# Kernel optimization log

Measured on AMD Instinct MI355X. Metric: run time of the kernel, lower is better.

The kernel has to match this reference:

```python
import jax, jax.numpy as jnp
import numpy as np

N_FEATURES = 40
H = 64
N_CLASSES = 3
N_NODES = 100000
N_EDGES = 3200000
THRESHOLD = 0.5


def setup_inputs() -> dict:
    key = jax.random.key(0)
    ks = jax.random.split(key, 8)
    x = jax.random.normal(ks[0], (N_NODES, N_FEATURES), dtype=jnp.float32)
    edge_index = jax.random.randint(ks[1], (2, N_EDGES), 0, N_NODES, dtype=jnp.int64)
    s1 = 1.0 / np.sqrt(N_FEATURES)
    s2 = 1.0 / np.sqrt(H)
    W1 = jax.random.uniform(ks[2], (N_FEATURES, H), jnp.float32, -s1, s1)
    b1 = jnp.zeros((H,), jnp.float32)
    Wf = jax.random.uniform(ks[3], (H, H), jnp.float32, -s2, s2)
    bf = jax.random.uniform(ks[4], (H,), jnp.float32, -s2, s2)
    W2 = jax.random.uniform(ks[5], (H, N_CLASSES), jnp.float32, -s2, s2)
    b2 = jnp.zeros((N_CLASSES,), jnp.float32)
    ethical_filter = jnp.ones((N_CLASSES,), jnp.float32)
    return {"x": x, "edge_index": edge_index, "W1": W1, "b1": b1,
            "Wf": Wf, "bf": bf, "W2": W2, "b2": b2,
            "ethical_filter": ethical_filter}


def _gcn_conv(x, W, b, src, dst, n_nodes):
    # PyG GCNConv: add self-loops, symmetric normalization, src->dst aggregate.
    h = x @ W                                   # [N, F_out]
    loop = jnp.arange(n_nodes, dtype=src.dtype)
    s = jnp.concatenate([src, loop])            # [E+N]
    d = jnp.concatenate([dst, loop])
    deg = jnp.zeros((n_nodes,), h.dtype).at[d].add(1.0)
    dinv = jax.lax.rsqrt(deg)                   # deg >= 1 due to self-loops
    norm = dinv[s] * dinv[d]                    # [E+N]
    msg = h[s] * norm[:, None]                  # gather + scale
    out = jnp.zeros((n_nodes, h.shape[1]), h.dtype).at[d].add(msg)
    return out + b


def reference(x, edge_index, W1, b1, Wf, bf, W2, b2, ethical_filter):
    n = x.shape[0]
    src, dst = edge_index[0], edge_index[1]
    h = jax.nn.relu(_gcn_conv(x, W1, b1, src, dst, n))
    # SpikingNeuron: mem = fc(h); spike = (mem >= threshold).float()
    spike = (h @ Wf + bf >= THRESHOLD).astype(x.dtype)
    out = _gcn_conv(spike, W2, b2, src, dst, n)
    return out * ethical_filter
```

## Files before the change

### kernel.cpp

```cpp
#include <hip/hip_runtime.h>

#define NF 40
#define NF4 10
#define H  64
#define NC 3
#define BK 256
#define CAP 10240
#define MAXNBK 512
#define SMASK 0xFFFFFu
#define NSLC 16
#define SSH 13

typedef float floatx4 __attribute__((ext_vector_type(4)));

__global__ void k_zero(int* __restrict__ p, int n) {
    int i = blockIdx.x * blockDim.x + threadIdx.x;
    if (i < n) p[i] = 0;
}

__global__ __launch_bounds__(1024) void k_bin(const int* __restrict__ src,
                                              const int* __restrict__ dst,
                                              int* __restrict__ gcur,
                                              unsigned* __restrict__ staging,
                                              int ne, int nbk) {
    __shared__ int lh[MAXNBK];
    __shared__ int lcur[MAXNBK];
    int t = threadIdx.x;
    for (int b = t; b < nbk; b += 1024) lh[b] = 0;
    __syncthreads();
    int gtid = blockIdx.x * 1024 + t;
    int NT = gridDim.x * 1024;
    int bk[13]; unsigned ed[13];
    #pragma unroll
    for (int u = 0; u < 13; ++u) {
        int i = gtid + u * NT;
        bool v = (i < ne);
        int dv = v ? dst[i] : 0;
        int sv = v ? src[i] : 0;
        bk[u] = v ? (dv >> 8) : -1;
        ed[u] = ((unsigned)(dv & 255) << 20) | (unsigned)sv;
        if (v) atomicAdd(&lh[dv >> 8], 1);
    }
    for (int i = gtid + 13 * NT; i < ne; i += NT)
        atomicAdd(&lh[dst[i] >> 8], 1);
    __syncthreads();
    for (int b = t; b < nbk; b += 1024)
        lcur[b] = lh[b] ? atomicAdd(&gcur[b], lh[b]) : 0;
    __syncthreads();
    #pragma unroll
    for (int u = 0; u < 13; ++u) {
        if (bk[u] >= 0) {
            int p = atomicAdd(&lcur[bk[u]], 1);
            staging[(size_t)bk[u] * CAP + p] = ed[u];
        }
    }
    for (int i = gtid + 13 * NT; i < ne; i += NT) {
        int dv = dst[i], sv = src[i]; int b = dv >> 8;
        int p = atomicAdd(&lcur[b], 1);
        staging[(size_t)b * CAP + p] = ((unsigned)(dv & 255) << 20) | (unsigned)sv;
    }
}

__global__ __launch_bounds__(512) void k_sort(unsigned* __restrict__ staging,
                                              const int* __restrict__ gcur,
                                              int* __restrict__ rs, int* __restrict__ rl,
                                              float* __restrict__ dinv, int n) {
    __shared__ unsigned buf[CAP];
    __shared__ int cnt[BK * NSLC];
    __shared__ int tsum[512];
    int b = blockIdx.x, t = threadIdx.x;
    int ebase = b * CAP;
    int rlen = gcur[b];
    for (int j = t; j < rlen; j += 512) buf[j] = staging[ebase + j];
    for (int i = t; i < BK * NSLC; i += 512) cnt[i] = 0;
    __syncthreads();
    for (int j = t; j < rlen; j += 512) {
        unsigned e = buf[j];
        int key = ((int)(e >> 20) << 4) | (int)((e & SMASK) >> SSH);
        atomicAdd(&cnt[key], 1);
    }
    __syncthreads();
    int base8 = t * 8;
    int loc[8]; int run = 0;
    #pragma unroll
    for (int i = 0; i < 8; ++i) { loc[i] = run; run += cnt[base8 + i]; }
    tsum[t] = run;
    __syncthreads();
    for (int off = 1; off < 512; off <<= 1) {
        int a = (t >= off) ? tsum[t - off] : 0;
        __syncthreads();
        tsum[t] += a;
        __syncthreads();
    }
    int texcl = tsum[t] - run;
    #pragma unroll
    for (int i = 0; i < 8; ++i) cnt[base8 + i] = texcl + loc[i];
    __syncthreads();
    if (t < BK) {
        int node = b * BK + t;
        int st0 = cnt[t * NSLC];
        int en0 = (t == BK - 1) ? rlen : cnt[(t + 1) * NSLC];
        int deg = en0 - st0;
        if (node < n) {
            rs[node] = ebase + st0;
            rl[node] = deg;
            dinv[node] = rsqrtf((float)(deg + 1));
        }
    }
    __syncthreads();
    for (int j = t; j < rlen; j += 512) {
        unsigned e = buf[j];
        int key = ((int)(e >> 20) << 4) | (int)((e & SMASK) >> SSH);
        int p = atomicAdd(&cnt[key], 1);
        staging[ebase + p] = e;
    }
}

__global__ __launch_bounds__(256) void k_pull1(
        const unsigned* __restrict__ st, const int* __restrict__ rs,
        const int* __restrict__ rl, const float* __restrict__ dinv,
        const float4* __restrict__ x4, float* __restrict__ ax, int n) {
    __shared__ float4 red[4][64];
    int t = threadIdx.x;
    int w = t >> 6, lane = t & 63;
    int d = blockIdx.x * 4 + w;
    if (d >= n) return;
    int g = lane / 10, f = lane - g * 10;
    int beg = rs[d], len = rl[d];
    float dd = dinv[d];
    float4 acc = make_float4(0.f, 0.f, 0.f, 0.f);
    if (g < 6) {
        int j = beg + g, end = beg + len;
        for (; j + 6 < end; j += 12) {
            unsigned eA = __builtin_nontemporal_load(st + j);
            unsigned eB = __builtin_nontemporal_load(st + j + 6);
            int sA = (int)(eA & SMASK), sB = (int)(eB & SMASK);
            float wA = dinv[sA], wB = dinv[sB];
            float4 a4 = x4[sA * NF4 + f];
            float4 b4 = x4[sB * NF4 + f];
            acc.x += a4.x * wA + b4.x * wB;
            acc.y += a4.y * wA + b4.y * wB;
            acc.z += a4.z * wA + b4.z * wB;
            acc.w += a4.w * wA + b4.w * wB;
        }
        if (j < end) {
            unsigned e = __builtin_nontemporal_load(st + j);
            int s = (int)(e & SMASK);
            float wv = dinv[s];
            float4 v = x4[s * NF4 + f];
            acc.x += v.x * wv; acc.y += v.y * wv;
            acc.z += v.z * wv; acc.w += v.w * wv;
        }
    }
    red[w][lane] = acc;
    if (lane < NF4) {
        float4 tot = red[w][lane];
        #pragma unroll
        for (int gg = 1; gg < 6; ++gg) {
            float4 r = red[w][gg * 10 + lane];
            tot.x += r.x; tot.y += r.y; tot.z += r.z; tot.w += r.w;
        }
        float4 self = x4[d * NF4 + lane];
        floatx4 o;
        o.x = dd * (tot.x + self.x * dd);
        o.y = dd * (tot.y + self.y * dd);
        o.z = dd * (tot.z + self.z * dd);
        o.w = dd * (tot.w + self.w * dd);
        __builtin_nontemporal_store(o, (floatx4*)(ax + (size_t)d * NF + 4 * lane));
    }
}

__global__ __launch_bounds__(256, 2) void k_node(
        const float4* __restrict__ ax4,
        const float* __restrict__ W1, const float* __restrict__ b1,
        const float* __restrict__ Wf, const float* __restrict__ bf,
        const float* __restrict__ W2, const float* __restrict__ dinv,
        float4* __restrict__ s2sp4, int n) {
    __shared__ float lW1[NF * H];
    __shared__ float lWf[H * H];
    __shared__ float hT[4][H * 32];
    int t = threadIdx.x, w = t >> 6, lane = t & 63;
    int r = lane & 7, c = lane >> 3;

    for (int i = t; i < NF * H; i += 256) lW1[i] = W1[i];
    for (int i = t; i < H * H;  i += 256) lWf[i] = Wf[i];
    __syncthreads();

    int nb0 = (blockIdx.x * 4 + w) * 32;
    if (nb0 >= n) return;
    int cnt = min(32, n - nb0);

    float bb[8], bfv[8], w2s[8][3];
    #pragma unroll
    for (int j = 0; j < 8; ++j) {
        bb[j]  = b1[8 * c + j];
        bfv[j] = bf[8 * c + j];
        w2s[j][0] = W2[(8 * c + j) * NC + 0];
        w2s[j][1] = W2[(8 * c + j) * NC + 1];
        w2s[j][2] = W2[(8 * c + j) * NC + 2];
    }

    float* axT = &hT[w][0];
    #pragma unroll
    for (int i = 0; i < 5; ++i) {
        int idx = lane + 64 * i;
        int no = idx / NF4, q = idx - no * NF4;
        float4 a = make_float4(0.f, 0.f, 0.f, 0.f);
        if (no < cnt) a = ax4[(size_t)(nb0 + no) * NF4 + q];
        axT[(4 * q + 0) * 32 + no] = a.x;
        axT[(4 * q + 1) * 32 + no] = a.y;
        axT[(4 * q + 2) * 32 + no] = a.z;
        axT[(4 * q + 3) * 32 + no] = a.w;
    }

    float acc[4][8];
    #pragma unroll
    for (int i = 0; i < 4; ++i)
        #pragma unroll
        for (int j = 0; j < 8; ++j) acc[i][j] = bb[j];
    for (int k = 0; k < NF; ++k) {
        float4 a   = *(const float4*)&axT[k * 32 + 4 * r];
        float4 blo = *(const float4*)&lW1[k * H + 8 * c];
        float4 bhi = *(const float4*)&lW1[k * H + 8 * c + 4];
        float av[4] = {a.x, a.y, a.z, a.w};
        float bv[8] = {blo.x, blo.y, blo.z, blo.w, bhi.x, bhi.y, bhi.z, bhi.w};
        #pragma unroll
        for (int i = 0; i < 4; ++i)
            #pragma unroll
            for (int j = 0; j < 8; ++j) acc[i][j] = fmaf(av[i], bv[j], acc[i][j]);
    }
    #pragma unroll
    for (int j = 0; j < 8; ++j) {
        float4 hv = make_float4(fmaxf(acc[0][j], 0.f), fmaxf(acc[1][j], 0.f),
                                fmaxf(acc[2][j], 0.f), fmaxf(acc[3][j], 0.f));
        *(float4*)&hT[w][(8 * c + j) * 32 + 4 * r] = hv;
    }

    float acc2[4][8];
    #pragma unroll
    for (int i = 0; i < 4; ++i)
        #pragma unroll
        for (int j = 0; j < 8; ++j) acc2[i][j] = bfv[j];
    for (int k = 0; k < H; ++k) {
        float4 a   = *(const float4*)&hT[w][k * 32 + 4 * r];
        float4 blo = *(const float4*)&lWf[k * H + 8 * c];
        float4 bhi = *(const float4*)&lWf[k * H + 8 * c + 4];
        float av[4] = {a.x, a.y, a.z, a.w};
        float bv[8] = {blo.x, blo.y, blo.z, blo.w, bhi.x, bhi.y, bhi.z, bhi.w};
        #pragma unroll
        for (int i = 0; i < 4; ++i)
            #pragma unroll
            for (int j = 0; j < 8; ++j) acc2[i][j] = fmaf(av[i], bv[j], acc2[i][j]);
    }

    float p0[4], p1[4], p2[4];
    #pragma unroll
    for (int i = 0; i < 4; ++i) { p0[i] = 0.f; p1[i] = 0.f; p2[i] = 0.f; }
    #pragma unroll
    for (int i = 0; i < 4; ++i)
        #pragma unroll
        for (int j = 0; j < 8; ++j) {
            float s = (acc2[i][j] >= 0.5f) ? 1.f : 0.f;
            p0[i] = fmaf(s, w2s[j][0], p0[i]);
            p1[i] = fmaf(s, w2s[j][1], p1[i]);
            p2[i] = fmaf(s, w2s[j][2], p2[i]);
        }
    #pragma unroll
    for (int off = 8; off < 64; off <<= 1) {
        #pragma unroll
        for (int i = 0; i < 4; ++i) {
            p0[i] += __shfl_xor(p0[i], off);
            p1[i] += __shfl_xor(p1[i], off);
            p2[i] += __shfl_xor(p2[i], off);
        }
    }
    if (c == 0) {
        #pragma unroll
        for (int i = 0; i < 4; ++i) {
            int no = 4 * r + i;
            if (no < cnt) {
                int node = nb0 + no;
                float di = dinv[node];
                s2sp4[node] = make_float4(p0[i] * di, p1[i] * di, p2[i] * di, 0.f);
            }
        }
    }
}

__global__ __launch_bounds__(256) void k_pull2(
        const unsigned* __restrict__ st, const int* __restrict__ rs,
        const int* __restrict__ rl, const float* __restrict__ dinv,
        const float4* __restrict__ s2sp4, const float* __restrict__ b2,
        const float* __restrict__ ef, float* __restrict__ out, int n) {
    int t = threadIdx.x;
    int w = t >> 6, lane = t & 63;
    int d = blockIdx.x * 4 + w;
    if (d >= n) return;
    int beg = rs[d], end = beg + rl[d];
    float a0 = 0.f, a1 = 0.f, a2 = 0.f;
    for (int j = beg + lane; j < end; j += 64) {
        unsigned e = __builtin_nontemporal_load(st + j);
        float4 v = s2sp4[e & SMASK];
        a0 += v.x; a1 += v.y; a2 += v.z;
    }
    for (int off = 32; off; off >>= 1) {
        a0 += __shfl_down(a0, off);
        a1 += __shfl_down(a1, off);
        a2 += __shfl_down(a2, off);
    }
    if (lane == 0) {
        float dd = dinv[d];
        float4 self = s2sp4[d];
        out[d * NC + 0] = (dd * (a0 + self.x) + b2[0]) * ef[0];
        out[d * NC + 1] = (dd * (a1 + self.y) + b2[1]) * ef[1];
        out[d * NC + 2] = (dd * (a2 + self.z) + b2[2]) * ef[2];
    }
}

extern "C" void kernel_launch(void* const* d_in, const int* in_sizes, int n_in,
                              void* d_out, int out_size, void* d_ws, size_t ws_size,
                              hipStream_t stream) {
    const float* x  = (const float*)d_in[0];
    const int*   ei = (const int*)d_in[1];
    const float* W1 = (const float*)d_in[2];
    const float* b1 = (const float*)d_in[3];
    const float* Wf = (const float*)d_in[4];
    const float* bf = (const float*)d_in[5];
    const float* W2 = (const float*)d_in[6];
    const float* b2 = (const float*)d_in[7];
    const float* ef = (const float*)d_in[8];

    int n  = in_sizes[0] / NF;
    int ne = in_sizes[1] / 2;
    const int* src = ei;
    const int* dst = ei + ne;
    int nbk = (n + BK - 1) >> 8;

    auto al = [](size_t v) { return (v + 255) & ~(size_t)255; };
    char* ws = (char*)d_ws;
    size_t off = 0;
    unsigned* staging = (unsigned*)(ws + off); off += al((size_t)nbk * CAP * 4);
    float*    axbuf   = (float*)(ws + off);    off += al((size_t)n * NF * 4);
    float*    s2sp    = (float*)(ws + off);    off += al((size_t)n * 4 * 4);
    float*    dinv    = (float*)(ws + off);    off += al((size_t)n * 4);
    int*      rsb     = (int*)(ws + off);      off += al((size_t)n * 4);
    int*      rlb     = (int*)(ws + off);      off += al((size_t)n * 4);
    int*      gcur    = (int*)(ws + off);      off += al((size_t)MAXNBK * 4);
    float* out = (float*)d_out;

    k_zero <<<2, 256, 0, stream>>>(gcur, MAXNBK);
    k_bin  <<<256, 1024, 0, stream>>>(src, dst, gcur, staging, ne, nbk);
    k_sort <<<nbk, 512, 0, stream>>>(staging, gcur, rsb, rlb, dinv, n);
    k_pull1<<<(n + 3) / 4, 256, 0, stream>>>(staging, rsb, rlb, dinv,
                                             (const float4*)x, axbuf, n);
    k_node <<<(n + 127) / 128, 256, 0, stream>>>(
        (const float4*)axbuf, W1, b1, Wf, bf, W2, dinv, (float4*)s2sp, n);
    k_pull2<<<(n + 3) / 4, 256, 0, stream>>>(staging, rsb, rlb, dinv, (const float4*)s2sp,
                                             b2, ef, out, n);
}
```

Measured before the change: 231.0 us.

## Locally sort edges per block before binning and drop src sub-sort

Rewrites the binning kernel so each block takes a contiguous chunk of edges, counting-sorts it by destination bucket in shared memory, then writes each bucket's run to staging, giving more coalesced scattered writes. The per-bucket sort kernel no longer sub-sorts by source slice, which removes the extra source-locality ordering and its bigger scan. Nontemporal loads and stores in the pull kernels become ordinary accesses. The trade-off is possibly worse gather locality in the pull kernels, since edges within a node are no longer grouped by source range.

```diff
diff --git a/kernel.cpp b/kernel.cpp
--- a/kernel.cpp
+++ b/kernel.cpp
@@ -8,56 +8,59 @@
 #define CAP 10240
 #define MAXNBK 512
 #define SMASK 0xFFFFFu
-#define NSLC 16
-#define SSH 13
-
-typedef float floatx4 __attribute__((ext_vector_type(4)));
+#define EPB 6400
 
 __global__ void k_zero(int* __restrict__ p, int n) {
     int i = blockIdx.x * blockDim.x + threadIdx.x;
     if (i < n) p[i] = 0;
 }
 
-__global__ __launch_bounds__(1024) void k_bin(const int* __restrict__ src,
+__global__ __launch_bounds__(512) void k_bin2(const int* __restrict__ src,
                                               const int* __restrict__ dst,
                                               int* __restrict__ gcur,
                                               unsigned* __restrict__ staging,
                                               int ne, int nbk) {
-    __shared__ int lh[MAXNBK];
-    __shared__ int lcur[MAXNBK];
+    __shared__ unsigned sorted[EPB];
+    __shared__ unsigned short sbk[EPB];
+    __shared__ int cnt[MAXNBK];
+    __shared__ int tsum[MAXNBK];
+    __shared__ int lstart[MAXNBK];
+    __shared__ int gbase[MAXNBK];
+    __shared__ int cur[MAXNBK];
     int t = threadIdx.x;
-    for (int b = t; b < nbk; b += 1024) lh[b] = 0;
-    __syncthreads();
-    int gtid = blockIdx.x * 1024 + t;
-    int NT = gridDim.x * 1024;
-    int bk[13]; unsigned ed[13];
-    #pragma unroll
-    for (int u = 0; u < 13; ++u) {
-        int i = gtid + u * NT;
-        bool v = (i < ne);
-        int dv = v ? dst[i] : 0;
-        int sv = v ? src[i] : 0;
-        bk[u] = v ? (dv >> 8) : -1;
-        ed[u] = ((unsigned)(dv & 255) << 20) | (unsigned)sv;
-        if (v) atomicAdd(&lh[dv >> 8], 1);
-    }
-    for (int i = gtid + 13 * NT; i < ne; i += NT)
-        atomicAdd(&lh[dst[i] >> 8], 1);
-    __syncthreads();
-    for (int b = t; b < nbk; b += 1024)
-        lcur[b] = lh[b] ? atomicAdd(&gcur[b], lh[b]) : 0;
-    __syncthreads();
-    #pragma unroll
-    for (int u = 0; u < 13; ++u) {
-        if (bk[u] >= 0) {
-            int p = atomicAdd(&lcur[bk[u]], 1);
-            staging[(size_t)bk[u] * CAP + p] = ed[u];
-        }
-    }
-    for (int i = gtid + 13 * NT; i < ne; i += NT) {
-        int dv = dst[i], sv = src[i]; int b = dv >> 8;
-        int p = atomicAdd(&lcur[b], 1);
-        staging[(size_t)b * CAP + p] = ((unsigned)(dv & 255) << 20) | (unsigned)sv;
+    int e0 = blockIdx.x * EPB;
+    int m = min(EPB, ne - e0);
+    if (m <= 0) return;
+
+    for (int b = t; b < MAXNBK; b += 512) cnt[b] = 0;
+    __syncthreads();
+    for (int j = t; j < m; j += 512)
+        atomicAdd(&cnt[dst[e0 + j] >> 8], 1);
+    __syncthreads();
+    int val = (t < nbk) ? cnt[t] : 0;
+    tsum[t] = val;
+    __syncthreads();
+    for (int off = 1; off < 512; off <<= 1) {
+        int a = (t >= off) ? tsum[t - off] : 0;
+        __syncthreads();
+        tsum[t] += a;
+        __syncthreads();
+    }
+    lstart[t] = tsum[t] - val;
+    cur[t] = tsum[t] - val;
+    if (t < nbk) gbase[t] = val ? atomicAdd(&gcur[t], val) : 0;
+    __syncthreads();
+    for (int j = t; j < m; j += 512) {
+        int d = dst[e0 + j], s = src[e0 + j];
+        int b = d >> 8;
+        int p = atomicAdd(&cur[b], 1);
+        sorted[p] = ((unsigned)(d & 255) << 20) | (unsigned)s;
+        sbk[p] = (unsigned short)b;
+    }
+    __syncthreads();
+    for (int j = t; j < m; j += 512) {
+        int b = sbk[j];
+        staging[(size_t)b * CAP + gbase[b] + (j - lstart[b])] = sorted[j];
     }
 }
 
@@ -66,52 +69,41 @@
                                               int* __restrict__ rs, int* __restrict__ rl,
                                               float* __restrict__ dinv, int n) {
     __shared__ unsigned buf[CAP];
-    __shared__ int cnt[BK * NSLC];
-    __shared__ int tsum[512];
+    __shared__ int cnt[BK];
+    __shared__ int scn[BK];
+    __shared__ int cur[BK];
     int b = blockIdx.x, t = threadIdx.x;
     int ebase = b * CAP;
     int rlen = gcur[b];
     for (int j = t; j < rlen; j += 512) buf[j] = staging[ebase + j];
-    for (int i = t; i < BK * NSLC; i += 512) cnt[i] = 0;
+    if (t < BK) cnt[t] = 0;
+    __syncthreads();
+    for (int j = t; j < rlen; j += 512)
+        atomicAdd(&cnt[buf[j] >> 20], 1);
+    __syncthreads();
+    if (t < BK) scn[t] = cnt[t];
+    __syncthreads();
+    for (int off = 1; off < BK; off <<= 1) {
+        int a = (t < BK && t >= off) ? scn[t - off] : 0;
+        __syncthreads();
+        if (t < BK) scn[t] += a;
+        __syncthreads();
+    }
+    if (t < BK) {
+        int deg = cnt[t];
+        int excl = scn[t] - deg;
+        cur[t] = excl;
+        int node = b * BK + t;
+        if (node < n) {
+            rs[node] = ebase + excl;
+            rl[node] = deg;
+            dinv[node] = rsqrtf((float)(deg + 1));
+        }
+    }
     __syncthreads();
     for (int j = t; j < rlen; j += 512) {
         unsigned e = buf[j];
-        int key = ((int)(e >> 20) << 4) | (int)((e & SMASK) >> SSH);
-        atomicAdd(&cnt[key], 1);
-    }
-    __syncthreads();
-    int base8 = t * 8;
-    int loc[8]; int run = 0;
-    #pragma unroll
-    for (int i = 0; i < 8; ++i) { loc[i] = run; run += cnt[base8 + i]; }
-    tsum[t] = run;
-    __syncthreads();
-    for (int off = 1; off < 512; off <<= 1) {
-        int a = (t >= off) ? tsum[t - off] : 0;
-        __syncthreads();
-        tsum[t] += a;
-        __syncthreads();
-    }
-    int texcl = tsum[t] - run;
-    #pragma unroll
-    for (int i = 0; i < 8; ++i) cnt[base8 + i] = texcl + loc[i];
-    __syncthreads();
-    if (t < BK) {
-        int node = b * BK + t;
-        int st0 = cnt[t * NSLC];
-        int en0 = (t == BK - 1) ? rlen : cnt[(t + 1) * NSLC];
-        int deg = en0 - st0;
-        if (node < n) {
-            rs[node] = ebase + st0;
-            rl[node] = deg;
-            dinv[node] = rsqrtf((float)(deg + 1));
-        }
-    }
-    __syncthreads();
-    for (int j = t; j < rlen; j += 512) {
-        unsigned e = buf[j];
-        int key = ((int)(e >> 20) << 4) | (int)((e & SMASK) >> SSH);
-        int p = atomicAdd(&cnt[key], 1);
+        int p = atomicAdd(&cur[e >> 20], 1);
         staging[ebase + p] = e;
     }
 }
@@ -119,7 +111,7 @@
 __global__ __launch_bounds__(256) void k_pull1(
         const unsigned* __restrict__ st, const int* __restrict__ rs,
         const int* __restrict__ rl, const float* __restrict__ dinv,
-        const float4* __restrict__ x4, float* __restrict__ ax, int n) {
+        const float4* __restrict__ x4, float4* __restrict__ ax4, int n) {
     __shared__ float4 red[4][64];
     int t = threadIdx.x;
     int w = t >> 6, lane = t & 63;
@@ -132,8 +124,7 @@
     if (g < 6) {
         int j = beg + g, end = beg + len;
         for (; j + 6 < end; j += 12) {
-            unsigned eA = __builtin_nontemporal_load(st + j);
-            unsigned eB = __builtin_nontemporal_load(st + j + 6);
+            unsigned eA = st[j], eB = st[j + 6];
             int sA = (int)(eA & SMASK), sB = (int)(eB & SMASK);
             float wA = dinv[sA], wB = dinv[sB];
             float4 a4 = x4[sA * NF4 + f];
@@ -144,7 +135,7 @@
             acc.w += a4.w * wA + b4.w * wB;
         }
         if (j < end) {
-            unsigned e = __builtin_nontemporal_load(st + j);
+            unsigned e = st[j];
             int s = (int)(e & SMASK);
             float wv = dinv[s];
             float4 v = x4[s * NF4 + f];
@@ -161,12 +152,12 @@
             tot.x += r.x; tot.y += r.y; tot.z += r.z; tot.w += r.w;
         }
         float4 self = x4[d * NF4 + lane];
-        floatx4 o;
+        float4 o;
         o.x = dd * (tot.x + self.x * dd);
         o.y = dd * (tot.y + self.y * dd);
         o.z = dd * (tot.z + self.z * dd);
         o.w = dd * (tot.w + self.w * dd);
-        __builtin_nontemporal_store(o, (floatx4*)(ax + (size_t)d * NF + 4 * lane));
+        ax4[d * NF4 + lane] = o;
     }
 }
 
@@ -299,8 +290,7 @@
     int beg = rs[d], end = beg + rl[d];
     float a0 = 0.f, a1 = 0.f, a2 = 0.f;
     for (int j = beg + lane; j < end; j += 64) {
-        unsigned e = __builtin_nontemporal_load(st + j);
-        float4 v = s2sp4[e & SMASK];
+        float4 v = s2sp4[st[j] & SMASK];
         a0 += v.x; a1 += v.y; a2 += v.z;
     }
     for (int off = 32; off; off >>= 1) {
@@ -348,11 +338,13 @@
     int*      gcur    = (int*)(ws + off);      off += al((size_t)MAXNBK * 4);
     float* out = (float*)d_out;
 
+    int binblocks = (ne + EPB - 1) / EPB;
+
     k_zero <<<2, 256, 0, stream>>>(gcur, MAXNBK);
-    k_bin  <<<256, 1024, 0, stream>>>(src, dst, gcur, staging, ne, nbk);
+    k_bin2 <<<binblocks, 512, 0, stream>>>(src, dst, gcur, staging, ne, nbk);
     k_sort <<<nbk, 512, 0, stream>>>(staging, gcur, rsb, rlb, dinv, n);
     k_pull1<<<(n + 3) / 4, 256, 0, stream>>>(staging, rsb, rlb, dinv,
-                                             (const float4*)x, axbuf, n);
+                                             (const float4*)x, (float4*)axbuf, n);
     k_node <<<(n + 127) / 128, 256, 0, stream>>>(
         (const float4*)axbuf, W1, b1, Wf, bf, W2, dinv, (float4*)s2sp, n);
     k_pull2<<<(n + 3) / 4, 256, 0, stream>>>(staging, rsb, rlb, dinv, (const float4*)s2sp,
```

After: 214.2 us. -7.3%, faster.
